# Optimization experiments

Hardware: AMD Instinct MI355X
Metric: run time of the kernel (lower is better)

Reference implementation:

```python
import jax, jax.numpy as jnp
import numpy as np

B, T, C = 4, 1536, 1536
H, DK, DV = 8, 64, 192
NB = 32  # num_basis per feature class: 192 // (2*3)
MIN_HALF_LIFE = 3.0


def pos_feats_all(distances, seq_len, nb=NB):
    """Enformer positional basis: [exponential, central_mask, gamma], asymmetric.
    distances: int array [L]; returns [L, 6*nb] float32."""
    pos = jnp.abs(distances).astype(jnp.float32)[:, None]  # [L,1]
    sl = jnp.float32(seq_len)
    # exponential
    max_range = jnp.log(sl) / jnp.log(2.0)
    half_life = jnp.power(2.0, jnp.linspace(MIN_HALF_LIFE, max_range, nb))  # [nb]
    f_exp = jnp.exp(-jnp.log(2.0) / half_life * pos)
    # central mask
    widths = jnp.power(2.0, jnp.arange(1, nb + 1, dtype=jnp.float32)) - 1.0
    f_cm = (widths > pos).astype(jnp.float32)
    # gamma
    stddev = sl / (2.0 * nb)
    start_mean = sl / nb
    mean = jnp.linspace(start_mean, sl, nb)
    conc = (mean / stddev) ** 2
    rate = mean / stddev ** 2
    log_unnorm = (conc - 1.0) * jnp.log(pos) - rate * pos  # log(0)=-inf -> exp=0 at pos=0
    log_norm = jax.lax.lgamma(conc) - conc * jnp.log(rate)
    prob = jnp.exp(log_unnorm - log_norm) + 1e-8
    f_gm = prob / jnp.max(prob, axis=0, keepdims=True)
    emb = jnp.concatenate([f_exp, f_cm, f_gm], axis=-1)  # [L, 3*nb]
    sign = jnp.sign(distances).astype(jnp.float32)[:, None]
    return jnp.concatenate([emb, sign * emb], axis=-1)  # [L, 6*nb]


def relative_shift(x):
    """x: [B,H,T,2T-1] -> [B,H,T,T] via the Transformer-XL shift trick."""
    b, h, t, l = x.shape  # l = 2t-1
    x = jnp.pad(x, ((0, 0), (0, 0), (0, 0), (1, 0)))  # [b,h,t,2t]
    x = x.reshape(b, h, l + 1, t)[:, :, 1:, :].reshape(b, h, t, l)
    return x[..., :t]


def setup_inputs() -> dict:
    key = jax.random.key(0)
    ks = jax.random.split(key, 10)
    def dense(k, fi, fo):  # VarianceScaling(scale=2.0)-like init
        return (jax.random.normal(k, (fi, fo), jnp.float32) * np.sqrt(2.0 / fi)).astype(jnp.float32)
    return {
        "x": jax.random.normal(ks[0], (B, T, C), jnp.float32),
        "W_q": dense(ks[1], C, H * DK),
        "W_k": dense(ks[2], C, H * DK),
        "W_v": dense(ks[3], C, H * DV),
        "W_rel_k": dense(ks[4], 6 * NB, H * DK),
        "W_out": dense(ks[5], H * DV, H * DV),
        "b_out": jnp.zeros((H * DV,), jnp.float32),
        "r_w_bias": jax.random.normal(ks[6], (1, H, 1, DK), jnp.float32) * np.sqrt(2.0 / DK),
        "r_r_bias": jax.random.normal(ks[7], (1, H, 1, DK), jnp.float32) * np.sqrt(2.0 / DK),
    }


def reference(x, W_q, W_k, W_v, W_rel_k, W_out, b_out, r_w_bias, r_r_bias):
    b, t, _ = x.shape
    def heads(w, d):  # [b,t,H*d] -> [b,H,t,d]
        return (x @ w).reshape(b, t, H, d).transpose(0, 2, 1, 3)
    Q = heads(W_q, DK) * (DK ** -0.5)  # scaling applied before biases
    K = heads(W_k, DK)
    V = heads(W_v, DV)
    distances = jnp.arange(-t + 1, t)  # [2t-1]
    pe = pos_feats_all(distances, t)  # [2t-1, 6*NB]
    rK = (pe @ W_rel_k).reshape(2 * t - 1, H, DK).transpose(1, 0, 2)  # [H, 2t-1, DK]
    content = jnp.einsum('bhqd,bhkd->bhqk', Q + r_w_bias, K)
    rel = jnp.einsum('bhqd,hld->bhql', Q + r_r_bias, rK)  # [b,H,t,2t-1]
    logits = content + relative_shift(rel)
    attn = jax.nn.softmax(logits, axis=-1)
    out = jnp.einsum('bhqk,bhkd->bhqd', attn, V)  # [b,H,t,DV]
    out = out.transpose(0, 2, 1, 3).reshape(b, t, H * DV)
    return out @ W_out + b_out
```

## Files before the change

kernel.cpp:

```cpp
#include <hip/hip_runtime.h>
#include <hip/hip_bf16.h>
#include <math.h>

#define BB 4
#define TT 1536
#define CC 1536
#define HH 8
#define DKk 64
#define DVv 192
#define NBASIS 32
#define LREL 3071
#define MROWS 6144

typedef short short8 __attribute__((ext_vector_type(8)));
typedef float floatx4 __attribute__((ext_vector_type(4)));

static __device__ inline short f2bf(float f) {
  __hip_bfloat16 h = __float2bfloat16(f);
  return *reinterpret_cast<short*>(&h);
}

static __device__ inline void gload_lds16(const __hip_bfloat16* g, __hip_bfloat16* l) {
  __builtin_amdgcn_global_load_lds(
      (const __attribute__((address_space(1))) unsigned int*)g,
      (__attribute__((address_space(3))) unsigned int*)l, 16, 0, 0);
}

__global__ void detect_kernel(const void* __restrict__ x, int* __restrict__ flag) {
  if (threadIdx.x == 0 && blockIdx.x == 0) {
    const __hip_bfloat16* h = (const __hip_bfloat16*)x;
    int cnt = 0;
    for (int i = 0; i < 64; ++i) {
      float v = fabsf((float)h[2 * i]);
      if (v > 1e-5f && v < 256.0f) cnt++;
    }
    *flag = (cnt >= 32) ? 1 : 0;
  }
}

__global__ __launch_bounds__(256) void convert_kernel(const void* __restrict__ src,
                                                      float* __restrict__ dst, int n,
                                                      const int* __restrict__ flag) {
  const int i = blockIdx.x * 256 + threadIdx.x;
  if (i >= n) return;
  if (*flag) dst[i] = (float)((const __hip_bfloat16*)src)[i];
  else       dst[i] = ((const float*)src)[i];
}

__global__ __launch_bounds__(256) void convbf_kernel(const void* __restrict__ src,
                                                     __hip_bfloat16* __restrict__ dst, int n,
                                                     const int* __restrict__ flag) {
  const int i = blockIdx.x * 256 + threadIdx.x;
  if (i >= n) return;
  if (*flag) dst[i] = ((const __hip_bfloat16*)src)[i];
  else       dst[i] = __float2bfloat16(((const float*)src)[i]);
}

__global__ __launch_bounds__(256) void wt_kernel(const void* __restrict__ src,
                                                 __hip_bfloat16* __restrict__ dst,
                                                 int K, int N, const int* __restrict__ flag) {
  __shared__ __hip_bfloat16 tile[64][68];
  const int tid = threadIdx.x;
  const int k0 = blockIdx.y * 64, n0 = blockIdx.x * 64;
  const bool bf = (*flag != 0);
  {
    const int r = tid >> 2, c0 = (tid & 3) * 16;
    if (bf) {
      const __hip_bfloat16* sp = (const __hip_bfloat16*)src + (size_t)(k0 + r) * N + n0 + c0;
#pragma unroll
      for (int u = 0; u < 16; ++u) tile[r][c0 + u] = sp[u];
    } else {
      const float* sp = (const float*)src + (size_t)(k0 + r) * N + n0 + c0;
#pragma unroll
      for (int u = 0; u < 16; ++u) tile[r][c0 + u] = __float2bfloat16(sp[u]);
    }
  }
  __syncthreads();
  {
    const int nr = tid >> 2, c0 = (tid & 3) * 16;
    __hip_bfloat16* dp = dst + (size_t)(n0 + nr) * K + k0 + c0;
#pragma unroll
    for (int u = 0; u < 16; ++u) dp[u] = tile[c0 + u][nr];
  }
}

__global__ void gmax_kernel(double* __restrict__ gmax) {
  const int j = blockIdx.x;
  const double mean = 48.0 + 1488.0 * (double)j / 31.0;
  const double conc = (mean / 24.0) * (mean / 24.0);
  const double rate = mean / 576.0;
  const double log_norm = lgamma(conc) - conc * log(rate);
  double mx = 1e-8;
  for (int pos = 1 + threadIdx.x; pos <= 1535; pos += 256) {
    double p = exp((conc - 1.0) * log((double)pos) - rate * (double)pos - log_norm) + 1e-8;
    mx = fmax(mx, p);
  }
  __shared__ double red[256];
  red[threadIdx.x] = mx;
  __syncthreads();
  for (int s = 128; s > 0; s >>= 1) {
    if (threadIdx.x < s) red[threadIdx.x] = fmax(red[threadIdx.x], red[threadIdx.x + s]);
    __syncthreads();
  }
  if (threadIdx.x == 0) gmax[j] = red[0];
}

__global__ void pe_kernel(float* __restrict__ pe, const double* __restrict__ gmax) {
  const int l = blockIdx.x;
  const int f = threadIdx.x;
  const int dist = l - (TT - 1);
  const int pos = dist < 0 ? -dist : dist;
  const int base = f % 96;
  const int cls = base / 32;
  const int j = base % 32;
  double v;
  if (cls == 0) {
    const double max_range = log(1536.0) / log(2.0);
    const double e = 3.0 + (max_range - 3.0) * (double)j / 31.0;
    const double hl = exp2(e);
    v = exp2(-(double)pos / hl);
  } else if (cls == 1) {
    const double width = exp2((double)(j + 1)) - 1.0;
    v = (width > (double)pos) ? 1.0 : 0.0;
  } else {
    const double mean = 48.0 + 1488.0 * (double)j / 31.0;
    const double conc = (mean / 24.0) * (mean / 24.0);
    const double rate = mean / 576.0;
    double p;
    if (pos == 0) {
      p = 1e-8;
    } else {
      const double log_norm = lgamma(conc) - conc * log(rate);
      p = exp((conc - 1.0) * log((double)pos) - rate * (double)pos - log_norm) + 1e-8;
    }
    v = p / gmax[j];
  }
  float out = (float)v;
  if (f >= 96) {
    float sgn = (dist > 0) ? 1.f : (dist < 0 ? -1.f : 0.f);
    out *= sgn;
  }
  pe[(size_t)l * 192 + f] = out;
}

__global__ __launch_bounds__(512) void relk_kernel(const float* __restrict__ pe,
                                                   const float* __restrict__ Wrk,
                                                   __hip_bfloat16* __restrict__ rKl) {
  __shared__ float pes[8][192];
  const int l0 = blockIdx.x * 8;
  const int nrows = (LREL - l0) < 8 ? (LREL - l0) : 8;
  const int tid = threadIdx.x;
  for (int idx = tid; idx < nrows * 192; idx += 512) {
    int r = idx / 192, f = idx % 192;
    pes[r][f] = pe[(size_t)(l0 + r) * 192 + f];
  }
  __syncthreads();
  float acc[8] = {0.f, 0.f, 0.f, 0.f, 0.f, 0.f, 0.f, 0.f};
  for (int f = 0; f < 192; ++f) {
    float w = Wrk[(size_t)f * 512 + tid];
#pragma unroll
    for (int r = 0; r < 8; ++r) acc[r] += pes[r][f] * w;
  }
  const int h = tid >> 6, d = tid & 63;
  for (int r = 0; r < nrows; ++r)
    rKl[((size_t)h * LREL + (l0 + r)) * 64 + d] = __float2bfloat16(acc[r]);
}

template <int MODE, bool BIAS>
__global__ __launch_bounds__(256) void gemm_mfma(const __hip_bfloat16* __restrict__ A,
                                                 const __hip_bfloat16* __restrict__ Bt,
                                                 void* __restrict__ Cout,
                                                 void* __restrict__ Cout2,
                                                 const float* __restrict__ bias,
                                                 int M, int N, int K,
                                                 const int* __restrict__ flag) {
  __shared__ __align__(16) __hip_bfloat16 As[128 * 32];
  __shared__ __align__(16) __hip_bfloat16 Bs[128 * 32];
  const int tid = threadIdx.x;
  const int w = tid >> 6, lane = tid & 63;
  const int quad = lane >> 4, l16 = lane & 15;
  const int wm = w >> 1, wn = w & 1;
  const int row0 = blockIdx.y * 128, col0 = blockIdx.x * 128;

  const floatx4 vzero = {0.f, 0.f, 0.f, 0.f};
  floatx4 acc[4][4];
#pragma unroll
  for (int i = 0; i < 4; ++i)
#pragma unroll
    for (int j = 0; j < 4; ++j) acc[i][j] = vzero;

  const int sr = lane >> 2;
  const int sc = (lane & 3) * 8;
  const __hip_bfloat16* ag0 = A + (size_t)(row0 + w * 32 + sr) * K + sc;
  const __hip_bfloat16* ag1 = A + (size_t)(row0 + w * 32 + 16 + sr) * K + sc;
  const __hip_bfloat16* bg0 = Bt + (size_t)(col0 + w * 32 + sr) * K + sc;
  const __hip_bfloat16* bg1 = Bt + (size_t)(col0 + w * 32 + 16 + sr) * K + sc;
  __hip_bfloat16* as0 = As + w * 32 * 32;
  __hip_bfloat16* as1 = As + (w * 32 + 16) * 32;
  __hip_bfloat16* bs0 = Bs + w * 32 * 32;
  __hip_bfloat16* bs1 = Bs + (w * 32 + 16) * 32;

  for (int k0 = 0; k0 < K; k0 += 32) {
    __syncthreads();
    gload_lds16(ag0 + k0, as0);
    gload_lds16(ag1 + k0, as1);
    gload_lds16(bg0 + k0, bs0);
    gload_lds16(bg1 + k0, bs1);
    __syncthreads();
    short8 aF[4], bF[4];
#pragma unroll
    for (int mt = 0; mt < 4; ++mt)
      aF[mt] = *(const short8*)(As + (wm * 64 + mt * 16 + l16) * 32 + quad * 8);
#pragma unroll
    for (int nt = 0; nt < 4; ++nt)
      bF[nt] = *(const short8*)(Bs + (wn * 64 + nt * 16 + l16) * 32 + quad * 8);
#pragma unroll
    for (int mt = 0; mt < 4; ++mt)
#pragma unroll
      for (int nt = 0; nt < 4; ++nt)
        acc[mt][nt] = __builtin_amdgcn_mfma_f32_16x16x32_bf16(aF[mt], bF[nt], acc[mt][nt], 0, 0, 0);
  }

  const bool obf = (MODE == 2) ? (*flag != 0) : false;
#pragma unroll
  for (int mt = 0; mt < 4; ++mt) {
#pragma unroll
    for (int r = 0; r < 4; ++r) {
      const int row = row0 + wm * 64 + mt * 16 + quad * 4 + r;
#pragma unroll
      for (int nt = 0; nt < 4; ++nt) {
        const int col = col0 + wn * 64 + nt * 16 + l16;
        float v = acc[mt][nt][r];
        if (BIAS) v += bias[col];
        if (MODE == 0) {
          ((float*)Cout)[(size_t)row * N + col] = v;
        } else if (MODE == 1) {
          ((__hip_bfloat16*)Cout)[(size_t)row * N + col] = __float2bfloat16(v);
        } else if (MODE == 2) {
          if (obf) ((__hip_bfloat16*)Cout)[(size_t)row * N + col] = __float2bfloat16(v);
          else     ((float*)Cout)[(size_t)row * N + col] = v;
        } else {
          if (col < 512)
            ((float*)Cout)[(size_t)row * 512 + col] = v;
          else
            ((__hip_bfloat16*)Cout2)[(size_t)row * 512 + (col - 512)] = __float2bfloat16(v);
        }
      }
    }
  }
}

__global__ __launch_bounds__(256) void kfrag_kernel(const __hip_bfloat16* __restrict__ Kbf,
                                                    __hip_bfloat16* __restrict__ Kfrag) {
  const int widx = blockIdx.x * 256 + threadIdx.x;
  const int lane = widx & 63;
  const int ks = (widx >> 6) & 1;
  const int kt = (widx >> 7) % 96;
  const int bh = (widx >> 7) / 96;
  const int b = bh >> 3, h = bh & 7;
  const __hip_bfloat16* src = Kbf + ((size_t)(b * TT + kt * 16 + (lane & 15))) * 512
                              + h * 64 + ks * 32 + (lane >> 4) * 8;
  *(uint4*)(Kfrag + (size_t)widx * 8) = *(const uint4*)src;
}

__global__ __launch_bounds__(256) void rkfrag_kernel(const __hip_bfloat16* __restrict__ rKl,
                                                     __hip_bfloat16* __restrict__ rKfrag) {
  const int widx = blockIdx.x * 256 + threadIdx.x;
  const int lane = widx & 63;
  const int ks = (widx >> 6) & 1;
  const int lt = (widx >> 7) % 192;
  const int h = (widx >> 7) / 192;
  int l = lt * 16 + (lane & 15);
  if (l > 3070) l = 3070;
  const __hip_bfloat16* src = rKl + ((size_t)h * LREL + l) * 64 + ks * 32 + (lane >> 4) * 8;
  *(uint4*)(rKfrag + (size_t)widx * 8) = *(const uint4*)src;
}

__global__ __launch_bounds__(256) void vfrag_kernel(const __hip_bfloat16* __restrict__ Vbf,
                                                    __hip_bfloat16* __restrict__ Vfrag) {
  int bid = blockIdx.x;
  int vt3 = bid % 3; int kb = (bid / 3) % 24; int h = (bid / 72) & 7; int b = bid / 576;
  const int bh = b * 8 + h;
  __shared__ __hip_bfloat16 tile[64][72];
  const int tid = threadIdx.x;
  {
    int r = tid >> 2, c0 = (tid & 3) * 16;
    const __hip_bfloat16* src = Vbf + (size_t)(b * TT + kb * 64 + r) * 1536 + h * 192 + vt3 * 64 + c0;
#pragma unroll
    for (int u = 0; u < 16; ++u) tile[r][c0 + u] = src[u];
  }
  __syncthreads();
#pragma unroll
  for (int u = 0; u < 2; ++u) {
    const int w512 = u * 256 + tid;
    const int vtl = w512 >> 7;
    const int ks = (w512 >> 6) & 1;
    const int ln = w512 & 63;
    const int qd = ln >> 4, s16 = ln & 15;
    union { uint4 u4; unsigned short us[8]; } pk;
#pragma unroll
    for (int j = 0; j < 8; ++j)
      pk.us[j] = *(const unsigned short*)&tile[ks * 32 + qd * 8 + j][vtl * 16 + s16];
    __hip_bfloat16* dst = Vfrag +
        (((size_t)(bh * 24 + kb) * 12 + vt3 * 4 + vtl) * 2 + ks) * 512 + (size_t)ln * 8;
    *(uint4*)dst = pk.u4;
  }
}

__global__ __launch_bounds__(256, 3) void attn_frag(
    const float* __restrict__ tmpQ,
    const float* __restrict__ rwb,
    const float* __restrict__ rrb,
    const __hip_bfloat16* __restrict__ Kfrag,
    const __hip_bfloat16* __restrict__ rKfrag,
    const __hip_bfloat16* __restrict__ Vfrag,
    __hip_bfloat16* __restrict__ O)
{
  const int tid = threadIdx.x;
  const int w = tid >> 6, lane = tid & 63;
  const int quad = lane >> 4, l16 = lane & 15;
  const int le8 = lane * 8;
  const int o = (blockIdx.x & 7) * 96 + (blockIdx.x >> 3);
  const int qt = o % 24;
  const int h = (o / 24) & 7;
  const int b = o / 192;
  const int bh = b * 8 + h;
  const int q0 = qt * 64;

  __shared__ __align__(16) char sm[50688];
  __hip_bfloat16* Klds  = (__hip_bfloat16*)sm;
  __hip_bfloat16* rKlds = (__hip_bfloat16*)(sm + 8192);
  __hip_bfloat16* Rbuf  = (__hip_bfloat16*)sm;
  __hip_bfloat16* Ptile = (__hip_bfloat16*)(sm + 16896);
  __hip_bfloat16* Vlds  = (__hip_bfloat16*)(sm + 26112);

  short8 aQw[2], aQr[2];
  {
    const int qrow = q0 + w * 16 + l16;
    const float* qp = tmpQ + (size_t)(b * TT + qrow) * 512 + h * 64;
#pragma unroll
    for (int ks = 0; ks < 2; ++ks) {
#pragma unroll
      for (int j = 0; j < 8; ++j) {
        const int d = ks * 32 + quad * 8 + j;
        const float qv = qp[d] * 0.125f;
        aQw[ks][j] = f2bf(qv + rwb[h * 64 + d]);
        aQr[ks][j] = f2bf(qv + rrb[h * 64 + d]);
      }
    }
  }

  const floatx4 vzero = {0.f, 0.f, 0.f, 0.f};
  floatx4 Oacc[12];
#pragma unroll
  for (int i = 0; i < 12; ++i) Oacc[i] = vzero;
  float mrow[4], lrow[4];
#pragma unroll
  for (int r = 0; r < 4; ++r) { mrow[r] = -INFINITY; lrow[r] = 0.f; }

  const __hip_bfloat16* kSrc = Kfrag + (size_t)bh * 98304 + le8;
  const __hip_bfloat16* rSrc = rKfrag + (size_t)h * 196608
                               + (size_t)((1472 - q0) >> 4) * 1024 + le8;
  const __hip_bfloat16* vSrc = Vfrag + (size_t)bh * 294912 + le8;

  const int jt0 = 3 - w;

  for (int k0 = 0; k0 < TT; k0 += 64) {
    __syncthreads();
    {
      const __hip_bfloat16* kIt = kSrc + (size_t)(k0 >> 4) * 1024;
      const __hip_bfloat16* rIt = rSrc + (size_t)(k0 >> 4) * 1024;
      const __hip_bfloat16* vIt = vSrc + (size_t)(k0 >> 6) * 12288;
      if (w == 0) {
#pragma unroll
        for (int i = 0; i < 8; ++i) gload_lds16(kIt + i * 512, Klds + i * 512);
#pragma unroll
        for (int i = 0; i < 4; ++i) gload_lds16(rIt + i * 512, rKlds + i * 512);
      } else if (w == 1) {
#pragma unroll
        for (int i = 4; i < 16; ++i) gload_lds16(rIt + i * 512, rKlds + i * 512);
      } else if (w == 2) {
#pragma unroll
        for (int i = 0; i < 12; ++i) gload_lds16(vIt + i * 512, Vlds + i * 512);
      } else {
#pragma unroll
        for (int i = 12; i < 24; ++i) gload_lds16(vIt + i * 512, Vlds + i * 512);
      }
    }
    __syncthreads();

    floatx4 S[4], R[5];
#pragma unroll
    for (int i = 0; i < 4; ++i) S[i] = vzero;
#pragma unroll
    for (int i = 0; i < 5; ++i) R[i] = vzero;

    __builtin_amdgcn_s_setprio(1);
#pragma unroll
    for (int kt = 0; kt < 4; ++kt) {
#pragma unroll
      for (int ks = 0; ks < 2; ++ks) {
        short8 bK = *(const short8*)(Klds + (kt * 2 + ks) * 512 + le8);
        S[kt] = __builtin_amdgcn_mfma_f32_16x16x32_bf16(aQw[ks], bK, S[kt], 0, 0, 0);
      }
    }
#pragma unroll
    for (int i = 0; i < 5; ++i) {
      const int jt = jt0 + i;
#pragma unroll
      for (int ks = 0; ks < 2; ++ks) {
        short8 bR = *(const short8*)(rKlds + (jt * 2 + ks) * 512 + le8);
        R[i] = __builtin_amdgcn_mfma_f32_16x16x32_bf16(aQr[ks], bR, R[i], 0, 0, 0);
      }
    }
    __builtin_amdgcn_s_setprio(0);
    __syncthreads();

#pragma unroll
    for (int i = 0; i < 5; ++i) {
      const int jt = jt0 + i;
#pragma unroll
      for (int r = 0; r < 4; ++r) {
        const int row = w * 16 + quad * 4 + r;
        Rbuf[row * 132 + jt * 16 + l16] = __float2bfloat16(R[i][r]);
      }
    }
#pragma unroll
    for (int kt = 0; kt < 4; ++kt) {
#pragma unroll
      for (int r = 0; r < 4; ++r) {
        const int row = w * 16 + quad * 4 + r;
        const int j = kt * 16 + l16 + 63 - row;
        S[kt][r] += (float)Rbuf[row * 132 + j];
      }
    }

    float alpha[4];
#pragma unroll
    for (int r = 0; r < 4; ++r) {
      float mx = fmaxf(fmaxf(S[0][r], S[1][r]), fmaxf(S[2][r], S[3][r]));
#pragma unroll
      for (int off = 8; off > 0; off >>= 1) mx = fmaxf(mx, __shfl_xor(mx, off));
      const float nm = fmaxf(mrow[r], mx);
      alpha[r] = __expf(mrow[r] - nm);
      mrow[r] = nm;
      float ps = 0.f;
#pragma unroll
      for (int kt = 0; kt < 4; ++kt) {
        const float p = __expf(S[kt][r] - nm);
        S[kt][r] = p;
        ps += p;
      }
#pragma unroll
      for (int off = 8; off > 0; off >>= 1) ps += __shfl_xor(ps, off);
      lrow[r] = lrow[r] * alpha[r] + ps;
    }
#pragma unroll
    for (int kt = 0; kt < 4; ++kt) {
#pragma unroll
      for (int r = 0; r < 4; ++r) {
        const int row = w * 16 + quad * 4 + r;
        Ptile[row * 72 + kt * 16 + l16] = __float2bfloat16(S[kt][r]);
      }
    }
#pragma unroll
    for (int vt = 0; vt < 12; ++vt)
#pragma unroll
      for (int r = 0; r < 4; ++r) Oacc[vt][r] *= alpha[r];

    short8 aP[2];
#pragma unroll
    for (int ks = 0; ks < 2; ++ks)
      aP[ks] = *(const short8*)(Ptile + (w * 16 + l16) * 72 + ks * 32 + quad * 8);

    __builtin_amdgcn_s_setprio(1);
#pragma unroll
    for (int vt = 0; vt < 12; ++vt) {
#pragma unroll
      for (int ks = 0; ks < 2; ++ks) {
        short8 bV = *(const short8*)(Vlds + (vt * 2 + ks) * 512 + le8);
        Oacc[vt] = __builtin_amdgcn_mfma_f32_16x16x32_bf16(aP[ks], bV, Oacc[vt], 0, 0, 0);
      }
    }
    __builtin_amdgcn_s_setprio(0);
  }

#pragma unroll
  for (int r = 0; r < 4; ++r) {
    const float inv = 1.f / lrow[r];
    const int qrow = q0 + w * 16 + quad * 4 + r;
    __hip_bfloat16* op = O + (size_t)(b * TT + qrow) * 1536 + h * 192;
#pragma unroll
    for (int vt = 0; vt < 12; ++vt)
      op[vt * 16 + l16] = __float2bfloat16(Oacc[vt][r] * inv);
  }
}

extern "C" void kernel_launch(void* const* d_in, const int* in_sizes, int n_in,
                              void* d_out, int out_size, void* d_ws, size_t ws_size,
                              hipStream_t stream) {
  const void* x     = d_in[0];
  const void* W_q   = d_in[1];
  const void* W_k   = d_in[2];
  const void* W_v   = d_in[3];
  const void* W_rel = d_in[4];
  const void* W_out = d_in[5];
  const void* b_out = d_in[6];
  const void* r_w_b = d_in[7];
  const void* r_r_b = d_in[8];

  float* ws = (float*)d_ws;
  int*    flag = (int*)d_ws;
  double* gmax = (double*)(ws + 16);
  float* pe    = ws + 16 + 64;
  float* WrelF = pe    + (size_t)LREL * 192;
  float* boutF = WrelF + (size_t)192 * 512;
  float* rwbF  = boutF + 1536;
  float* rrbF  = rwbF + 512;
  float* tmpQ  = rrbF + 512;
  __hip_bfloat16* xBf  = (__hip_bfloat16*)(tmpQ + (size_t)MROWS * 512);
  __hip_bfloat16* WqT  = xBf  + (size_t)MROWS * 1536;
  __hip_bfloat16* WkT  = WqT  + (size_t)512 * 1536;
  __hip_bfloat16* WvT  = WkT  + (size_t)512 * 1536;
  __hip_bfloat16* WoT  = WvT  + (size_t)1536 * 1536;
  __hip_bfloat16* Kbf  = WoT  + (size_t)1536 * 1536;
  __hip_bfloat16* Vbf  = Kbf  + (size_t)MROWS * 512;
  __hip_bfloat16* Vfrag= Vbf  + (size_t)MROWS * 1536;
  __hip_bfloat16* Obf  = Vfrag + (size_t)32 * 192 * 1536;
  __hip_bfloat16* rKl  = Obf  + (size_t)MROWS * 1536;
  char* endp = (char*)(rKl + (size_t)HH * LREL * 64);
  if (ws_size < (size_t)(endp - (char*)d_ws)) return;

  __hip_bfloat16* Kfrag  = xBf;
  __hip_bfloat16* rKfrag = xBf + (size_t)3145728;

  detect_kernel<<<1, 64, 0, stream>>>(x, flag);

  auto conv = [&](const void* src, float* dst, int n) {
    convert_kernel<<<(n + 255) / 256, 256, 0, stream>>>(src, dst, n, flag);
  };
  conv(W_rel, WrelF, 192 * 512);
  conv(b_out, boutF, 1536);
  conv(r_w_b, rwbF,  512);
  conv(r_r_b, rrbF,  512);

  convbf_kernel<<<(MROWS * 1536 + 255) / 256, 256, 0, stream>>>(x, xBf, MROWS * 1536, flag);

  wt_kernel<<<dim3(512 / 64, 1536 / 64), 256, 0, stream>>>(W_q, WqT, 1536, 512, flag);
  wt_kernel<<<dim3(512 / 64, 1536 / 64), 256, 0, stream>>>(W_k, WkT, 1536, 512, flag);
  wt_kernel<<<dim3(1536 / 64, 1536 / 64), 256, 0, stream>>>(W_v, WvT, 1536, 1536, flag);
  wt_kernel<<<dim3(1536 / 64, 1536 / 64), 256, 0, stream>>>(W_out, WoT, 1536, 1536, flag);

  gmax_kernel<<<32, 256, 0, stream>>>(gmax);
  pe_kernel<<<LREL, 192, 0, stream>>>(pe, gmax);
  relk_kernel<<<(LREL + 7) / 8, 512, 0, stream>>>(pe, WrelF, rKl);

  gemm_mfma<3, false><<<dim3(1024 / 128, MROWS / 128), 256, 0, stream>>>(
      xBf, WqT, tmpQ, Kbf, nullptr, MROWS, 1024, CC, flag);
  gemm_mfma<1, false><<<dim3(1536 / 128, MROWS / 128), 256, 0, stream>>>(
      xBf, WvT, Vbf, nullptr, nullptr, MROWS, 1536, CC, flag);

  kfrag_kernel<<<1536, 256, 0, stream>>>(Kbf, Kfrag);
  rkfrag_kernel<<<768, 256, 0, stream>>>(rKl, rKfrag);
  vfrag_kernel<<<2304, 256, 0, stream>>>(Vbf, Vfrag);

  attn_frag<<<768, 256, 0, stream>>>(tmpQ, rwbF, rrbF, Kfrag, rKfrag, Vfrag, Obf);

  gemm_mfma<2, true><<<dim3(1536 / 128, MROWS / 128), 256, 0, stream>>>(
      Obf, WoT, d_out, nullptr, boutF, MROWS, 1536, CC, flag);
}
```

Before: 468.4 us.

## Widen GEMM K-tile with swizzled LDS, fuse QKV GEMMs, split PV by columns

The bf16 GEMM now stages 64-wide K slices per iteration and uses an XOR-swizzled LDS layout. This halves the number of barriers per K loop and is meant to avoid LDS bank conflicts on fragment reads. The Q/K and V projections are merged into a single launch with N=2560 and a third output pointer; this assumes the V weight follows the Q/K weights contiguously in memory. In the attention kernel, each wave now computes a 48-column slice of the PV product for all 64 query rows instead of all 192 columns for its own 16 rows. The softmax rescale factors and row sums are shared through LDS, which adds a couple of extra barriers. The relative-position buffer is shrunk to a per-tile window, which lowers LDS use.

```diff
diff --git a/kernel.cpp b/kernel.cpp
--- a/kernel.cpp
+++ b/kernel.cpp
@@ -171,11 +171,12 @@
                                                  const __hip_bfloat16* __restrict__ Bt,
                                                  void* __restrict__ Cout,
                                                  void* __restrict__ Cout2,
+                                                 void* __restrict__ Cout3,
                                                  const float* __restrict__ bias,
                                                  int M, int N, int K,
                                                  const int* __restrict__ flag) {
-  __shared__ __align__(16) __hip_bfloat16 As[128 * 32];
-  __shared__ __align__(16) __hip_bfloat16 Bs[128 * 32];
+  __shared__ __align__(16) __hip_bfloat16 As[128 * 64];
+  __shared__ __align__(16) __hip_bfloat16 Bs[128 * 64];
   const int tid = threadIdx.x;
   const int w = tid >> 6, lane = tid & 63;
   const int quad = lane >> 4, l16 = lane & 15;
@@ -189,36 +190,37 @@
 #pragma unroll
     for (int j = 0; j < 4; ++j) acc[i][j] = vzero;
 
-  const int sr = lane >> 2;
-  const int sc = (lane & 3) * 8;
-  const __hip_bfloat16* ag0 = A + (size_t)(row0 + w * 32 + sr) * K + sc;
-  const __hip_bfloat16* ag1 = A + (size_t)(row0 + w * 32 + 16 + sr) * K + sc;
-  const __hip_bfloat16* bg0 = Bt + (size_t)(col0 + w * 32 + sr) * K + sc;
-  const __hip_bfloat16* bg1 = Bt + (size_t)(col0 + w * 32 + 16 + sr) * K + sc;
-  __hip_bfloat16* as0 = As + w * 32 * 32;
-  __hip_bfloat16* as1 = As + (w * 32 + 16) * 32;
-  __hip_bfloat16* bs0 = Bs + w * 32 * 32;
-  __hip_bfloat16* bs1 = Bs + (w * 32 + 16) * 32;
-
-  for (int k0 = 0; k0 < K; k0 += 32) {
-    __syncthreads();
-    gload_lds16(ag0 + k0, as0);
-    gload_lds16(ag1 + k0, as1);
-    gload_lds16(bg0 + k0, bs0);
-    gload_lds16(bg1 + k0, bs1);
-    __syncthreads();
-    short8 aF[4], bF[4];
-#pragma unroll
-    for (int mt = 0; mt < 4; ++mt)
-      aF[mt] = *(const short8*)(As + (wm * 64 + mt * 16 + l16) * 32 + quad * 8);
-#pragma unroll
-    for (int nt = 0; nt < 4; ++nt)
-      bF[nt] = *(const short8*)(Bs + (wn * 64 + nt * 16 + l16) * 32 + quad * 8);
-#pragma unroll
-    for (int mt = 0; mt < 4; ++mt)
+  const int sr = lane >> 3;
+  const int sg = (lane & 7) ^ sr;
+  const __hip_bfloat16* ag = A + (size_t)(row0 + w * 32 + sr) * K + sg * 8;
+  const __hip_bfloat16* bg = Bt + (size_t)(col0 + w * 32 + sr) * K + sg * 8;
+  __hip_bfloat16* as_ = As + w * 32 * 64;
+  __hip_bfloat16* bs_ = Bs + w * 32 * 64;
+
+  for (int k0 = 0; k0 < K; k0 += 64) {
+    __syncthreads();
+#pragma unroll
+    for (int i = 0; i < 4; ++i) {
+      gload_lds16(ag + (size_t)(i * 8) * K + k0, as_ + i * 8 * 64);
+      gload_lds16(bg + (size_t)(i * 8) * K + k0, bs_ + i * 8 * 64);
+    }
+    __syncthreads();
+#pragma unroll
+    for (int ks = 0; ks < 2; ++ks) {
+      const int xr = (((ks * 4 + quad) ^ (l16 & 7)) << 3);
+      short8 aF[4], bF[4];
+#pragma unroll
+      for (int mt = 0; mt < 4; ++mt)
+        aF[mt] = *(const short8*)(As + (wm * 64 + mt * 16 + l16) * 64 + xr);
 #pragma unroll
       for (int nt = 0; nt < 4; ++nt)
-        acc[mt][nt] = __builtin_amdgcn_mfma_f32_16x16x32_bf16(aF[mt], bF[nt], acc[mt][nt], 0, 0, 0);
+        bF[nt] = *(const short8*)(Bs + (wn * 64 + nt * 16 + l16) * 64 + xr);
+#pragma unroll
+      for (int mt = 0; mt < 4; ++mt)
+#pragma unroll
+        for (int nt = 0; nt < 4; ++nt)
+          acc[mt][nt] = __builtin_amdgcn_mfma_f32_16x16x32_bf16(aF[mt], bF[nt], acc[mt][nt], 0, 0, 0);
+    }
   }
 
   const bool obf = (MODE == 2) ? (*flag != 0) : false;
@@ -242,8 +244,10 @@
         } else {
           if (col < 512)
             ((float*)Cout)[(size_t)row * 512 + col] = v;
+          else if (col < 1024)
+            ((__hip_bfloat16*)Cout2)[(size_t)row * 512 + (col - 512)] = __float2bfloat16(v);
           else
-            ((__hip_bfloat16*)Cout2)[(size_t)row * 512 + (col - 512)] = __float2bfloat16(v);
+            ((__hip_bfloat16*)Cout3)[(size_t)row * 1536 + (col - 1024)] = __float2bfloat16(v);
         }
       }
     }
@@ -327,12 +331,14 @@
   const int bh = b * 8 + h;
   const int q0 = qt * 64;
 
-  __shared__ __align__(16) char sm[50688];
+  __shared__ __align__(16) char sm[49152];
   __hip_bfloat16* Klds  = (__hip_bfloat16*)sm;
   __hip_bfloat16* rKlds = (__hip_bfloat16*)(sm + 8192);
+  __hip_bfloat16* Vlds  = (__hip_bfloat16*)(sm + 24576);
   __hip_bfloat16* Rbuf  = (__hip_bfloat16*)sm;
-  __hip_bfloat16* Ptile = (__hip_bfloat16*)(sm + 16896);
-  __hip_bfloat16* Vlds  = (__hip_bfloat16*)(sm + 26112);
+  __hip_bfloat16* Ptile = (__hip_bfloat16*)(sm + 10752);
+  float* alphaS = (float*)(sm + 19968);
+  float* lrowS  = (float*)(sm + 20224);
 
   short8 aQw[2], aQr[2];
   {
@@ -418,11 +424,10 @@
 
 #pragma unroll
     for (int i = 0; i < 5; ++i) {
-      const int jt = jt0 + i;
 #pragma unroll
       for (int r = 0; r < 4; ++r) {
         const int row = w * 16 + quad * 4 + r;
-        Rbuf[row * 132 + jt * 16 + l16] = __float2bfloat16(R[i][r]);
+        Rbuf[row * 84 + i * 16 + l16] = __float2bfloat16(R[i][r]);
       }
     }
 #pragma unroll
@@ -430,8 +435,8 @@
 #pragma unroll
       for (int r = 0; r < 4; ++r) {
         const int row = w * 16 + quad * 4 + r;
-        const int j = kt * 16 + l16 + 63 - row;
-        S[kt][r] += (float)Rbuf[row * 132 + j];
+        const int cj = kt * 16 + l16 + 15 - quad * 4 - r;
+        S[kt][r] += (float)Rbuf[row * 84 + cj];
       }
     }
 
@@ -463,36 +468,59 @@
         Ptile[row * 72 + kt * 16 + l16] = __float2bfloat16(S[kt][r]);
       }
     }
-#pragma unroll
-    for (int vt = 0; vt < 12; ++vt)
-#pragma unroll
-      for (int r = 0; r < 4; ++r) Oacc[vt][r] *= alpha[r];
-
-    short8 aP[2];
-#pragma unroll
-    for (int ks = 0; ks < 2; ++ks)
-      aP[ks] = *(const short8*)(Ptile + (w * 16 + l16) * 72 + ks * 32 + quad * 8);
+    if (l16 == 0) {
+#pragma unroll
+      for (int r = 0; r < 4; ++r) alphaS[w * 16 + quad * 4 + r] = alpha[r];
+    }
+    __syncthreads();
+
+#pragma unroll
+    for (int qf = 0; qf < 4; ++qf) {
+      const floatx4 al = *(const floatx4*)(alphaS + qf * 16 + quad * 4);
+#pragma unroll
+      for (int vtl = 0; vtl < 3; ++vtl)
+#pragma unroll
+        for (int r = 0; r < 4; ++r) Oacc[qf * 3 + vtl][r] *= al[r];
+    }
+
+    short8 aP[4][2];
+#pragma unroll
+    for (int qf = 0; qf < 4; ++qf)
+#pragma unroll
+      for (int ks = 0; ks < 2; ++ks)
+        aP[qf][ks] = *(const short8*)(Ptile + (qf * 16 + l16) * 72 + ks * 32 + quad * 8);
 
     __builtin_amdgcn_s_setprio(1);
 #pragma unroll
-    for (int vt = 0; vt < 12; ++vt) {
+    for (int vtl = 0; vtl < 3; ++vtl) {
 #pragma unroll
       for (int ks = 0; ks < 2; ++ks) {
-        short8 bV = *(const short8*)(Vlds + (vt * 2 + ks) * 512 + le8);
-        Oacc[vt] = __builtin_amdgcn_mfma_f32_16x16x32_bf16(aP[ks], bV, Oacc[vt], 0, 0, 0);
+        short8 bV = *(const short8*)(Vlds + ((w * 3 + vtl) * 2 + ks) * 512 + le8);
+#pragma unroll
+        for (int qf = 0; qf < 4; ++qf)
+          Oacc[qf * 3 + vtl] = __builtin_amdgcn_mfma_f32_16x16x32_bf16(aP[qf][ks], bV, Oacc[qf * 3 + vtl], 0, 0, 0);
       }
     }
     __builtin_amdgcn_s_setprio(0);
   }
 
-#pragma unroll
-  for (int r = 0; r < 4; ++r) {
-    const float inv = 1.f / lrow[r];
-    const int qrow = q0 + w * 16 + quad * 4 + r;
-    __hip_bfloat16* op = O + (size_t)(b * TT + qrow) * 1536 + h * 192;
-#pragma unroll
-    for (int vt = 0; vt < 12; ++vt)
-      op[vt * 16 + l16] = __float2bfloat16(Oacc[vt][r] * inv);
+  if (l16 == 0) {
+#pragma unroll
+    for (int r = 0; r < 4; ++r) lrowS[w * 16 + quad * 4 + r] = lrow[r];
+  }
+  __syncthreads();
+#pragma unroll
+  for (int qf = 0; qf < 4; ++qf) {
+    const floatx4 lv = *(const floatx4*)(lrowS + qf * 16 + quad * 4);
+#pragma unroll
+    for (int r = 0; r < 4; ++r) {
+      const float inv = 1.f / lv[r];
+      const int qrow = q0 + qf * 16 + quad * 4 + r;
+      __hip_bfloat16* op = O + (size_t)(b * TT + qrow) * 1536 + h * 192 + w * 48;
+#pragma unroll
+      for (int vtl = 0; vtl < 3; ++vtl)
+        op[vtl * 16 + l16] = __float2bfloat16(Oacc[qf * 3 + vtl][r] * inv);
+    }
   }
 }
 
@@ -555,10 +583,8 @@
   pe_kernel<<<LREL, 192, 0, stream>>>(pe, gmax);
   relk_kernel<<<(LREL + 7) / 8, 512, 0, stream>>>(pe, WrelF, rKl);
 
-  gemm_mfma<3, false><<<dim3(1024 / 128, MROWS / 128), 256, 0, stream>>>(
-      xBf, WqT, tmpQ, Kbf, nullptr, MROWS, 1024, CC, flag);
-  gemm_mfma<1, false><<<dim3(1536 / 128, MROWS / 128), 256, 0, stream>>>(
-      xBf, WvT, Vbf, nullptr, nullptr, MROWS, 1536, CC, flag);
+  gemm_mfma<3, false><<<dim3(2560 / 128, MROWS / 128), 256, 0, stream>>>(
+      xBf, WqT, tmpQ, Kbf, Vbf, nullptr, MROWS, 2560, CC, flag);
 
   kfrag_kernel<<<1536, 256, 0, stream>>>(Kbf, Kfrag);
   rkfrag_kernel<<<768, 256, 0, stream>>>(rKl, rKfrag);
@@ -567,5 +593,5 @@
   attn_frag<<<768, 256, 0, stream>>>(tmpQ, rwbF, rrbF, Kfrag, rKfrag, Vfrag, Obf);
 
   gemm_mfma<2, true><<<dim3(1536 / 128, MROWS / 128), 256, 0, stream>>>(
-      Obf, WoT, d_out, nullptr, boutF, MROWS, 1536, CC, flag);
-}
+      Obf, WoT, d_out, nullptr, nullptr, boutF, MROWS, 1536, CC, flag);
+}
```

New measurement: 461.1 us. Within noise of the previous version (-1.5%).
